# Kernel optimization log

Hardware: AMD Instinct MI355X
Metric: run time of the kernel (lower is better)

## Reference

```python
import jax, jax.numpy as jnp
import numpy as np

B, T, DIM = 1, 1024, 1024
H = 8
QLR, KVLR = 768, 512
DNOPE, DROPE, DV = 128, 64, 128
DK = DNOPE + DROPE  # 192
EPS = 1e-5


def _rms(x, w):
    return x * jax.lax.rsqrt(jnp.mean(x * x, axis=-1, keepdims=True) + EPS) * w


def _l2norm(x):
    return x * jax.lax.rsqrt(jnp.sum(x * x, axis=-1, keepdims=True) + 1e-6)


def setup_inputs() -> dict:
    key = jax.random.key(0)
    ks = jax.random.split(key, 12)
    std = 0.02
    rnd = lambda k, shape: (jax.random.normal(k, shape, dtype=jnp.float32) * std)
    return {
        'x': jax.random.normal(ks[0], (B, T, DIM), dtype=jnp.float32),
        'cos': jax.random.normal(ks[1], (T, DROPE), dtype=jnp.float32),
        'sin': jax.random.normal(ks[2], (T, DROPE), dtype=jnp.float32),
        'wq_a': rnd(ks[3], (DIM, QLR)),
        'q_norm_w': jnp.ones((QLR,), dtype=jnp.float32),
        'wq_b': rnd(ks[4], (QLR, H * DK)),
        'wkv_a': rnd(ks[5], (DIM, KVLR + DROPE)),
        'kv_norm_w': jnp.ones((KVLR,), dtype=jnp.float32),
        'wkv_b': rnd(ks[6], (KVLR, H * (DNOPE + DV))),
        'wg_w': rnd(ks[7], (DIM, H * DK)),
        'wg_b': jnp.zeros((H * DK,), dtype=jnp.float32),
        'wb': rnd(ks[8], (DIM, H)),
        'wo': rnd(ks[9], (H * DV, DIM)),
    }


def _kda(q, k, v, g, beta):
    # q,k: [B,T,H,DK]; v: [B,T,H,DV]; g: [B,T,H,DK] (log-decay); beta: [B,T,H]
    q = _l2norm(q) * (DK ** -0.5)
    k = _l2norm(k)
    # time-major for scan
    qs = jnp.moveaxis(q, 1, 0)
    ks_ = jnp.moveaxis(k, 1, 0)
    vs = jnp.moveaxis(v, 1, 0)
    gs = jnp.moveaxis(g, 1, 0)
    bs = jnp.moveaxis(beta, 1, 0)

    def step(S, inp):
        q_t, k_t, v_t, g_t, b_t = inp  # [B,H,DK],[B,H,DK],[B,H,DV],[B,H,DK],[B,H]
        S = S * jnp.exp(g_t)[..., None]                       # per-key-dim decay
        u_t = b_t[..., None] * (v_t - jnp.einsum('bhk,bhkv->bhv', k_t, S))
        S = S + k_t[..., None] * u_t[..., None, :]            # rank-1 delta update
        o_t = jnp.einsum('bhk,bhkv->bhv', q_t, S)
        return S, o_t

    S0 = jnp.zeros((B, H, DK, DV), dtype=q.dtype)
    _, o = jax.lax.scan(step, S0, (qs, ks_, vs, gs, bs))
    return jnp.moveaxis(o, 0, 1)  # [B,T,H,DV]


def reference(x, cos, sin, wq_a, q_norm_w, wq_b, wkv_a, kv_norm_w, wkv_b, wg_w, wg_b, wb, wo):
    # cos/sin are accepted but unused, matching the original forward body.
    q = (_rms(x @ wq_a, q_norm_w) @ wq_b).reshape(B, T, H, DK)
    kv_all = x @ wkv_a
    kv_c, k_pe = kv_all[..., :KVLR], kv_all[..., KVLR:]       # [B,T,KVLR],[B,T,DROPE]
    kv = (_rms(kv_c, kv_norm_w) @ wkv_b).reshape(B, T, H, DNOPE + DV)
    k_nope, v = kv[..., :DNOPE], kv[..., DNOPE:]
    k = jnp.concatenate(
        [k_nope, jnp.broadcast_to(k_pe[:, :, None, :], (B, T, H, DROPE))], axis=-1)
    g = jax.nn.log_sigmoid(x @ wg_w + wg_b).reshape(B, T, H, DK)
    beta = jax.nn.sigmoid(x @ wb).reshape(B, T, H)
    o = _kda(q, k, v, g, beta)
    o = jnp.nan_to_num(o, nan=0.0, posinf=10000.0, neginf=-10000.0)
    return o.reshape(B, T, H * DV) @ wo
```

## Files before the change

### kernel.cpp

```cpp
#include <hip/hip_runtime.h>
#include <hip/hip_bf16.h>
#include <math.h>

#define TT 1024
#define DIM 1024
#define HH 8
#define QLR 768
#define KVLR 512
#define DNOPE 128
#define DROPE 64
#define DV 128
#define DK 192
#define HDK (HH*DK)
#define HKV (HH*(DNOPE+DV))

#define OY   0
#define OQ   3072
#define OC   6144
#define OPL  9984
#define OU   10240
#define OLAM 12288
#define PABLK 12480

typedef __attribute__((ext_vector_type(8))) short short8;
typedef __attribute__((ext_vector_type(4))) float f32x4;

__device__ __forceinline__ unsigned short f2bf_rn(float f) {
    unsigned u = __float_as_uint(f);
    unsigned lsb = (u >> 16) & 1u;
    u += 0x7fffu + lsb;
    return (unsigned short)(u >> 16);
}
__device__ __forceinline__ float bf2f(unsigned short h) {
    return __uint_as_float(((unsigned)h) << 16);
}

__global__ __launch_bounds__(256) void wconv(
    const float* __restrict__ W0, unsigned short* __restrict__ H0,
    unsigned short* __restrict__ L0, int K0, int N0, int T0,
    const float* __restrict__ W1, unsigned short* __restrict__ H1,
    unsigned short* __restrict__ L1, int K1, int N1, int T1,
    const float* __restrict__ W2, unsigned short* __restrict__ H2,
    unsigned short* __restrict__ L2, int K2, int N2, int T2)
{
    __shared__ float Ls[64][65];
    int bx = blockIdx.x;
    const float* W; unsigned short* H; unsigned short* L; int K, N;
    if (bx < T0)           { W = W0; H = H0; L = L0; K = K0; N = N0; }
    else if (bx < T0 + T1) { bx -= T0; W = W1; H = H1; L = L1; K = K1; N = N1; }
    else                   { bx -= T0 + T1; W = W2; H = H2; L = L2; K = K2; N = N2; }

    const int NT = N >> 6;
    const int kt = bx / NT, nt = bx - kt * NT;
    const int k0 = kt * 64, n0 = nt * 64;
    const int tid = threadIdx.x;
    const int r = tid >> 2, c = (tid & 3) * 16;

#pragma unroll
    for (int i = 0; i < 4; i++)
        *(float4*)&Ls[r][c + i * 4] =
            *(const float4*)&W[(size_t)(k0 + r) * N + n0 + c + i * 4];
    __syncthreads();

    const int nr = tid >> 2, kc = (tid & 3) * 16;
    unsigned short hb[16], lb[16];
#pragma unroll
    for (int j = 0; j < 16; j++) {
        float v = Ls[kc + j][nr];
        unsigned short h = f2bf_rn(v);
        hb[j] = h;
        lb[j] = f2bf_rn(v - bf2f(h));
    }
    size_t ob = (size_t)(n0 + nr) * K + k0 + kc;
    *(float4*)&H[ob]     = ((float4*)hb)[0];
    *(float4*)&H[ob + 8] = ((float4*)hb)[1];
    *(float4*)&L[ob]     = ((float4*)lb)[0];
    *(float4*)&L[ob + 8] = ((float4*)lb)[1];
}

__global__ __launch_bounds__(256) void aconv(
    const float* __restrict__ A, unsigned short* __restrict__ H,
    unsigned short* __restrict__ L)
{
    int i = (blockIdx.x * 256 + threadIdx.x) * 8;
    float4 v0 = *(const float4*)&A[i];
    float4 v1 = *(const float4*)&A[i + 4];
    float vv[8] = {v0.x, v0.y, v0.z, v0.w, v1.x, v1.y, v1.z, v1.w};
    unsigned short hb[8], lb[8];
#pragma unroll
    for (int j = 0; j < 8; j++) {
        unsigned short h = f2bf_rn(vv[j]);
        hb[j] = h;
        lb[j] = f2bf_rn(vv[j] - bf2f(h));
    }
    *(float4*)&H[i] = *(float4*)hb;
    *(float4*)&L[i] = *(float4*)lb;
}

__global__ __launch_bounds__(128) void gemm_bt(
    const unsigned short* __restrict__ Ah0, const unsigned short* __restrict__ Al0,
    const unsigned short* __restrict__ Bh0, const unsigned short* __restrict__ Bl0,
    float* __restrict__ C0, int K0, int N0, int T0,
    const unsigned short* __restrict__ Ah1, const unsigned short* __restrict__ Al1,
    const unsigned short* __restrict__ Bh1, const unsigned short* __restrict__ Bl1,
    float* __restrict__ C1, int K1, int N1, int T1,
    const unsigned short* __restrict__ Ah2, const unsigned short* __restrict__ Al2,
    const unsigned short* __restrict__ Bh2, const unsigned short* __restrict__ Bl2,
    float* __restrict__ C2, int K2, int N2, int T2)
{
    __shared__ unsigned short Ahs[64 * 40], Als[64 * 40];
    __shared__ unsigned short Bhs[64 * 40], Bls[64 * 40];

    int bx = blockIdx.x;
    const unsigned short *Ah, *Al, *Bh, *Bl; float* C; int K, N;
    if (bx < T0) {
        Ah = Ah0; Al = Al0; Bh = Bh0; Bl = Bl0; C = C0; K = K0; N = N0;
    } else if (bx < T0 + T1) {
        bx -= T0; Ah = Ah1; Al = Al1; Bh = Bh1; Bl = Bl1; C = C1; K = K1; N = N1;
    } else {
        bx -= T0 + T1; Ah = Ah2; Al = Al2; Bh = Bh2; Bl = Bl2; C = C2; K = K2; N = N2;
    }

    const int tid = threadIdx.x;
    const int w = tid >> 6, l = tid & 63;
    const int q = l >> 4, m16 = l & 15;
    const int bm = blockIdx.y * 64, bn = bx * 64;

    const int c0i = tid * 2, c1i = tid * 2 + 1;
    const int r0 = c0i >> 2, o0 = (c0i & 3) * 8;
    const int r1 = c1i >> 2, o1 = (c1i & 3) * 8;
    const unsigned short* pAh0 = Ah + (size_t)(bm + r0) * K + o0;
    const unsigned short* pAh1 = Ah + (size_t)(bm + r1) * K + o1;
    const unsigned short* pAl0 = Al + (size_t)(bm + r0) * K + o0;
    const unsigned short* pAl1 = Al + (size_t)(bm + r1) * K + o1;
    const unsigned short* pBh0 = Bh + (size_t)(bn + r0) * K + o0;
    const unsigned short* pBh1 = Bh + (size_t)(bn + r1) * K + o1;
    const unsigned short* pBl0 = Bl + (size_t)(bn + r0) * K + o0;
    const unsigned short* pBl1 = Bl + (size_t)(bn + r1) * K + o1;

    f32x4 acc[2][4];
#pragma unroll
    for (int i = 0; i < 2; i++)
#pragma unroll
        for (int j = 0; j < 4; j++)
            acc[i][j] = (f32x4){0.f, 0.f, 0.f, 0.f};

    float4 vAh0 = *(const float4*)pAh0, vAh1 = *(const float4*)pAh1;
    float4 vAl0 = *(const float4*)pAl0, vAl1 = *(const float4*)pAl1;
    float4 vBh0 = *(const float4*)pBh0, vBh1 = *(const float4*)pBh1;
    float4 vBl0 = *(const float4*)pBl0, vBl1 = *(const float4*)pBl1;

    for (int k0 = 0;; k0 += 32) {
        __syncthreads();
        *(float4*)&Ahs[r0 * 40 + o0] = vAh0; *(float4*)&Ahs[r1 * 40 + o1] = vAh1;
        *(float4*)&Als[r0 * 40 + o0] = vAl0; *(float4*)&Als[r1 * 40 + o1] = vAl1;
        *(float4*)&Bhs[r0 * 40 + o0] = vBh0; *(float4*)&Bhs[r1 * 40 + o1] = vBh1;
        *(float4*)&Bls[r0 * 40 + o0] = vBl0; *(float4*)&Bls[r1 * 40 + o1] = vBl1;
        __syncthreads();

        const bool more = (k0 + 32) < K;
        if (more) {
            const int kn = k0 + 32;
            vAh0 = *(const float4*)(pAh0 + kn); vAh1 = *(const float4*)(pAh1 + kn);
            vAl0 = *(const float4*)(pAl0 + kn); vAl1 = *(const float4*)(pAl1 + kn);
            vBh0 = *(const float4*)(pBh0 + kn); vBh1 = *(const float4*)(pBh1 + kn);
            vBl0 = *(const float4*)(pBl0 + kn); vBl1 = *(const float4*)(pBl1 + kn);
        }

        short8 fah[2], fal[2], fbh[4], fbl[4];
#pragma unroll
        for (int mt = 0; mt < 2; mt++) {
            const int row = w * 32 + mt * 16 + m16;
            fah[mt] = *(const short8*)&Ahs[row * 40 + q * 8];
            fal[mt] = *(const short8*)&Als[row * 40 + q * 8];
        }
#pragma unroll
        for (int nt = 0; nt < 4; nt++) {
            const int row = nt * 16 + m16;
            fbh[nt] = *(const short8*)&Bhs[row * 40 + q * 8];
            fbl[nt] = *(const short8*)&Bls[row * 40 + q * 8];
        }
#pragma unroll
        for (int mt = 0; mt < 2; mt++)
#pragma unroll
            for (int nt = 0; nt < 4; nt++) {
                acc[mt][nt] = __builtin_amdgcn_mfma_f32_16x16x32_bf16(
                    fah[mt], fbh[nt], acc[mt][nt], 0, 0, 0);
                acc[mt][nt] = __builtin_amdgcn_mfma_f32_16x16x32_bf16(
                    fah[mt], fbl[nt], acc[mt][nt], 0, 0, 0);
                acc[mt][nt] = __builtin_amdgcn_mfma_f32_16x16x32_bf16(
                    fal[mt], fbh[nt], acc[mt][nt], 0, 0, 0);
            }
        if (!more) break;
    }

#pragma unroll
    for (int mt = 0; mt < 2; mt++)
#pragma unroll
        for (int nt = 0; nt < 4; nt++) {
            const int mrow = bm + w * 32 + mt * 16 + q * 4;
            const int ncol = bn + nt * 16 + m16;
#pragma unroll
            for (int r = 0; r < 4; r++)
                C[(size_t)(mrow + r) * N + ncol] = acc[mt][nt][r];
        }
}

__global__ __launch_bounds__(256) void rmsnorm_bf(
    const float* __restrict__ in, int in_stride, const float* __restrict__ w,
    unsigned short* __restrict__ oh, unsigned short* __restrict__ ol,
    int ncols, float inv_n)
{
    const int t = blockIdx.x;
    const int tid = threadIdx.x;
    const float* row = in + (size_t)t * in_stride;
    float ss = 0.f;
    for (int c = tid; c < ncols; c += 256) { float v = row[c]; ss += v * v; }
#pragma unroll
    for (int m = 1; m < 64; m <<= 1) ss += __shfl_xor(ss, m);
    __shared__ float red[4];
    if ((tid & 63) == 0) red[tid >> 6] = ss;
    __syncthreads();
    float tot = red[0] + red[1] + red[2] + red[3];
    float scale = rsqrtf(tot * inv_n + 1e-5f);
    for (int c = tid; c < ncols; c += 256) {
        float v = row[c] * scale * w[c];
        unsigned short h = f2bf_rn(v);
        oh[(size_t)t * ncols + c] = h;
        ol[(size_t)t * ncols + c] = f2bf_rn(v - bf2f(h));
    }
}

__global__ __launch_bounds__(256) void logsig_relayout(
    const float* __restrict__ g, const float* __restrict__ bias,
    float* __restrict__ la_h)
{
    int i = blockIdx.x * 256 + threadIdx.x;
    int t = i / HDK, col = i - t * HDK;
    int h = col / DK, d = col - h * DK;
    float z = g[i] + bias[col];
    float la = fminf(z, 0.f) - log1pf(__expf(-fabsf(z)));
    la_h[((size_t)h * TT + t) * DK + d] = la;
}

__global__ __launch_bounds__(256) void beta_kernel(
    const float* __restrict__ x, const float* __restrict__ wb,
    float* __restrict__ beta)
{
    const int lane = threadIdx.x & 63, wv = threadIdx.x >> 6;
    const int p = blockIdx.x * 4 + wv;
    const int t = p >> 3, h = p & 7;
    const float* xr = x + (size_t)t * DIM;
    float s = 0.f;
    for (int e = lane; e < DIM; e += 64) s += xr[e] * wb[e * HH + h];
#pragma unroll
    for (int m = 1; m < 64; m <<= 1) s += __shfl_xor(s, m);
    if (lane == 0) beta[p] = 1.f / (1.f + expf(-s));
}

__global__ __launch_bounds__(256) void prep_qk(
    const float* __restrict__ qraw, const float* __restrict__ kvb,
    const float* __restrict__ kv_all, float* __restrict__ q_h,
    float* __restrict__ k_h)
{
    const int lane = threadIdx.x & 63, wv = threadIdx.x >> 6;
    const int p = blockIdx.x * 4 + wv;
    const int t = p >> 3, h = p & 7;

    const float* qrow = qraw + (size_t)t * HDK + h * DK;
    float q0 = qrow[lane], q1 = qrow[lane + 64], q2 = qrow[lane + 128];
    float ss = q0 * q0 + q1 * q1 + q2 * q2;
#pragma unroll
    for (int m = 1; m < 64; m <<= 1) ss += __shfl_xor(ss, m);
    float sc = rsqrtf(ss + 1e-6f) * 0.07216878364870323f;
    float* qo = q_h + ((size_t)h * TT + t) * DK;
    qo[lane] = q0 * sc; qo[lane + 64] = q1 * sc; qo[lane + 128] = q2 * sc;

    const float* knope = kvb + (size_t)t * HKV + h * (DNOPE + DV);
    float k0 = knope[lane], k1 = knope[lane + 64];
    float k2 = kv_all[(size_t)t * (KVLR + DROPE) + KVLR + lane];
    float ks = k0 * k0 + k1 * k1 + k2 * k2;
#pragma unroll
    for (int m = 1; m < 64; m <<= 1) ks += __shfl_xor(ks, m);
    float kc = rsqrtf(ks + 1e-6f);
    float* ko = k_h + ((size_t)h * TT + t) * DK;
    ko[lane] = k0 * kc; ko[lane + 64] = k1 * kc; ko[lane + 128] = k2 * kc;
}

__device__ __forceinline__ float dpp_xor1(float x) {
    return __int_as_float(__builtin_amdgcn_update_dpp(
        0, __float_as_int(x), 0xB1, 0xF, 0xF, false));
}
__device__ __forceinline__ float dpp_xor2(float x) {
    return __int_as_float(__builtin_amdgcn_update_dpp(
        0, __float_as_int(x), 0x4E, 0xF, 0xF, false));
}
__device__ __forceinline__ float red16(float x) {
    x += dpp_xor1(x);
    x += dpp_xor2(x);
    x += __int_as_float(__builtin_amdgcn_update_dpp(0, __float_as_int(x), 0x141, 0xF, 0xF, false));
    x += __int_as_float(__builtin_amdgcn_update_dpp(0, __float_as_int(x), 0x140, 0xF, 0xF, false));
    return x;
}

__device__ __forceinline__ void gl_lds16(const float* g, float* l) {
    __builtin_amdgcn_global_load_lds(
        (const __attribute__((address_space(1))) void*)g,
        (__attribute__((address_space(3))) void*)l, 16, 0, 0);
}
__device__ __forceinline__ void gl_lds4(const float* g, float* l) {
    __builtin_amdgcn_global_load_lds(
        (const __attribute__((address_space(1))) void*)g,
        (__attribute__((address_space(3))) void*)l, 4, 0, 0);
}

__global__ __launch_bounds__(256) void chunk_prep(
    const float* __restrict__ k_h, const float* __restrict__ la_h,
    const float* __restrict__ q_h, const float* __restrict__ kvb,
    const float* __restrict__ betab, float* __restrict__ pa)
{
    __shared__ float Ls[16][196];
    __shared__ float Ks[16][196];
    __shared__ float Qs[16][196];
    __shared__ float Ws[16][196];
    __shared__ float Xs[16][196];
    __shared__ float Ms[16][16];
    __shared__ float bs[16];

    const int tid = threadIdx.x;
    const int n = blockIdx.x >> 3, h = blockIdx.x & 7;
    const size_t g0 = ((size_t)h * TT + n * 16) * DK;
    float* blob = pa + (size_t)blockIdx.x * PABLK;

#pragma unroll
    for (int s = 0; s < 3; s++) {
        int off = (tid * 3 + s) * 4;
        int r = off / 192, c = off - r * 192;
        *(float4*)&Ks[r][c] = *(const float4*)(k_h + g0 + off);
        *(float4*)&Ls[r][c] = *(const float4*)(la_h + g0 + off);
        *(float4*)&Qs[r][c] = *(const float4*)(q_h + g0 + off);
    }
    if (tid < 16) bs[tid] = betab[(size_t)(n * 16 + tid) * HH + h];
    __syncthreads();

    if (tid < 192) {
        float g = 0.f;
#pragma unroll
        for (int i = 0; i < 16; i++) { g += Ls[i][tid]; Ls[i][tid] = g; }
    }
    __syncthreads();

#pragma unroll
    for (int s = 0; s < 12; s++) {
        int idx = s * 256 + tid;
        int i = idx / 192, d = idx - i * 192;
        float G = Ls[i][d];
        float eg = __expf(G), en = __expf(-G);
        float kk = Ks[i][d];
        Ws[i][d] = bs[i] * kk * eg;
        Qs[i][d] *= eg;
        Ks[i][d] = kk * en;
    }
    __syncthreads();

#pragma unroll
    for (int s = 0; s < 3; s++) {
        int off = (tid * 3 + s) * 4;
        int r = off / 192, c = off - r * 192;
        *(float4*)(blob + OQ + off) = *(const float4*)&Qs[r][c];
    }
    if (tid < 192) {
        float lam = __expf(Ls[15][tid]);
        blob[OLAM + tid] = lam;
#pragma unroll
        for (int j4 = 0; j4 < 4; j4++) {
            float4 v;
            v.x = Ks[j4 * 4 + 0][tid] * lam; v.y = Ks[j4 * 4 + 1][tid] * lam;
            v.z = Ks[j4 * 4 + 2][tid] * lam; v.w = Ks[j4 * 4 + 3][tid] * lam;
            *(float4*)(blob + OC + tid * 20 + j4 * 4) = v;
        }
        blob[OC + tid * 20 + 16] = 0.f; blob[OC + tid * 20 + 17] = 0.f;
        blob[OC + tid * 20 + 18] = 0.f; blob[OC + tid * 20 + 19] = 0.f;
    }
    {
        const int i = tid >> 4, j = tid & 15;
        float m = 0.f, p = 0.f;
#pragma unroll
        for (int d4 = 0; d4 < 48; d4++) {
            float4 w  = *(const float4*)&Ws[i][d4 * 4];
            float4 ka = *(const float4*)&Ks[j][d4 * 4];
            float4 qa = *(const float4*)&Qs[i][d4 * 4];
            m += w.x * ka.x + w.y * ka.y + w.z * ka.z + w.w * ka.w;
            p += qa.x * ka.x + qa.y * ka.y + qa.z * ka.z + qa.w * ka.w;
        }
        Ms[i][j] = (j < i) ? m : 0.f;
        blob[OPL + tid] = (j <= i) ? p : 0.f;
    }
    __syncthreads();

    float y[16], uu[16];
    const bool doY = (tid < 192);
    const bool doU = (tid >= 128);
    const int dcol = tid, ccol = tid - 128;
    if (doY) {
#pragma unroll
        for (int i = 0; i < 16; i++) y[i] = Ws[i][dcol];
#pragma unroll
        for (int i = 1; i < 16; i++)
#pragma unroll
            for (int j = 0; j < i; j++)
                y[i] = fmaf(-Ms[i][j], y[j], y[i]);
    }
    if (doU) {
#pragma unroll
        for (int i = 0; i < 16; i++)
            uu[i] = bs[i] * kvb[(size_t)(n * 16 + i) * HKV + h * (DNOPE + DV) + DNOPE + ccol];
#pragma unroll
        for (int i = 1; i < 16; i++)
#pragma unroll
            for (int j = 0; j < i; j++)
                uu[i] = fmaf(-Ms[i][j], uu[j], uu[i]);
    }
    if (doY) {
#pragma unroll
        for (int i = 0; i < 16; i++) Xs[i][dcol] = y[i];
    }
    __syncthreads();
#pragma unroll
    for (int s = 0; s < 3; s++) {
        int off = (tid * 3 + s) * 4;
        int r = off / 192, c = off - r * 192;
        *(float4*)(blob + OY + off) = *(const float4*)&Xs[r][c];
    }
    __syncthreads();
    if (doU) {
#pragma unroll
        for (int i = 0; i < 16; i++) Xs[i][ccol] = uu[i];
    }
    __syncthreads();
#pragma unroll
    for (int s = 0; s < 2; s++) {
        int off = (tid * 2 + s) * 4;
        int r = off / 128, c = off - r * 128;
        *(float4*)(blob + OU + off) = *(const float4*)&Xs[r][c];
    }
}

__global__ __launch_bounds__(256) void kda_chunk(
    const float* __restrict__ pa, unsigned short* __restrict__ obh,
    unsigned short* __restrict__ obl)
{
    __shared__ float Yb[3][3136];
    __shared__ float Qb[3][3136];
    __shared__ float Cb[3][3840];
    __shared__ float Pb[3][256];
    __shared__ float ubs[3][64];
    __shared__ float lbs[3][192];
    __shared__ float Ss[784];
    __shared__ float us[80];

    const int tid = threadIdx.x;
    const int w = tid >> 6, lane = tid & 63;
    const int h = blockIdx.x >> 5, cg = blockIdx.x & 31;
    const int c0 = cg * 4;

    const int dg  = tid & 15;
    const int ccg = (tid >> 4) & 1;
    const int tig = tid >> 5;

    auto stage = [&](int buf, int n) {
        const float* blob = pa + (size_t)(n * 8 + h) * PABLK;
        if (w == 0) {
            if (lane < 48)
#pragma unroll
                for (int r = 0; r < 16; r++)
                    gl_lds16(blob + OY + r * 192 + lane * 4, &Yb[buf][r * 196]);
        } else if (w == 1) {
            if (lane < 48)
#pragma unroll
                for (int r = 0; r < 16; r++)
                    gl_lds16(blob + OQ + r * 192 + lane * 4, &Qb[buf][r * 196]);
        } else if (w == 2) {
#pragma unroll
            for (int s = 0; s < 15; s++)
                gl_lds16(blob + OC + s * 256 + lane * 4, &Cb[buf][s * 256]);
        } else {
            gl_lds16(blob + OPL + lane * 4, &Pb[buf][0]);
            gl_lds4(blob + OU + (lane >> 2) * 128 + c0 + (lane & 3), &ubs[buf][0]);
            if (lane < 48)
                gl_lds16(blob + OLAM + lane * 4, &lbs[buf][0]);
        }
    };

    for (int idx = tid; idx < 784; idx += 256) Ss[idx] = 0.f;
    stage(0, 0);
    stage(1, 1);

    const int c2 = tid & 3, dseg = tid >> 2;

    int buf = 0;
    for (int n = 0; n < TT / 16; n++) {
        __syncthreads();

        if (n + 2 < TT / 16) {
            int b2 = buf + 2; if (b2 >= 3) b2 -= 3;
            stage(b2, n + 2);
        }

        const int dbase = dg * 12;
        float4 sv[2][3];
#pragma unroll
        for (int j = 0; j < 2; j++)
#pragma unroll
            for (int s = 0; s < 3; s++)
                sv[j][s] = *(const float4*)&Ss[(ccg * 2 + j) * 196 + dbase + s * 4];

        float py[2][2] = {{0.f, 0.f}, {0.f, 0.f}};
        float pq[2][2] = {{0.f, 0.f}, {0.f, 0.f}};
#pragma unroll
        for (int i = 0; i < 2; i++) {
            const float* Yr = &Yb[buf][(tig * 2 + i) * 196 + dbase];
            const float* Qr = &Qb[buf][(tig * 2 + i) * 196 + dbase];
#pragma unroll
            for (int s = 0; s < 3; s++) {
                float4 yv = *(const float4*)(Yr + s * 4);
                float4 qv = *(const float4*)(Qr + s * 4);
#pragma unroll
                for (int j = 0; j < 2; j++) {
                    float4 s4 = sv[j][s];
                    py[i][j] = fmaf(yv.x, s4.x, py[i][j]);
                    py[i][j] = fmaf(yv.y, s4.y, py[i][j]);
                    py[i][j] = fmaf(yv.z, s4.z, py[i][j]);
                    py[i][j] = fmaf(yv.w, s4.w, py[i][j]);
                    pq[i][j] = fmaf(qv.x, s4.x, pq[i][j]);
                    pq[i][j] = fmaf(qv.y, s4.y, pq[i][j]);
                    pq[i][j] = fmaf(qv.z, s4.z, pq[i][j]);
                    pq[i][j] = fmaf(qv.w, s4.w, pq[i][j]);
                }
            }
        }
        float zy[2][2], zq[2][2];
#pragma unroll
        for (int i = 0; i < 2; i++)
#pragma unroll
            for (int j = 0; j < 2; j++) {
                zy[i][j] = red16(py[i][j]);
                zq[i][j] = red16(pq[i][j]);
            }

        float uv[2][2];
#pragma unroll
        for (int i = 0; i < 2; i++)
#pragma unroll
            for (int j = 0; j < 2; j++)
                uv[i][j] = ubs[buf][(tig * 2 + i) * 4 + (ccg * 2 + j)] - zy[i][j];
        {
            const int m = dg >> 2;
            if ((dg & 3) == 0) {
                const int ii = m >> 1, jj = m & 1;
                float val = (m == 0) ? uv[0][0] : (m == 1) ? uv[0][1]
                          : (m == 2) ? uv[1][0] : uv[1][1];
                us[(ccg * 2 + jj) * 20 + (tig * 2 + ii)] = val;
            }
        }
        __syncthreads();

        {
            const int m = dg >> 2, qtr = dg & 3;
            const int ii = m >> 1, jj = m & 1;
            const int ti = tig * 2 + ii, cc = ccg * 2 + jj;
            float acc = 0.f;
            for (int j = qtr; j <= ti; j += 4)
                acc = fmaf(Pb[buf][ti * 16 + j], us[cc * 20 + j], acc);
            acc += dpp_xor1(acc);
            acc += dpp_xor2(acc);
            if (qtr == 0) {
                float zqv = (m == 0) ? zq[0][0] : (m == 1) ? zq[0][1]
                          : (m == 2) ? zq[1][0] : zq[1][1];
                float ov = zqv + acc;
                if (isnan(ov)) ov = 0.f;
                else if (isinf(ov)) ov = ov > 0.f ? 1e4f : -1e4f;
                size_t oi = (size_t)(n * 16 + ti) * (HH * DV) + h * DV + c0 + cc;
                unsigned short hb = f2bf_rn(ov);
                obh[oi] = hb;
                obl[oi] = f2bf_rn(ov - bf2f(hb));
            }
        }

        const float4* up = (const float4*)&us[c2 * 20];
        float4 u0 = up[0], u1 = up[1], u2v = up[2], u3 = up[3];
#pragma unroll
        for (int s = 0; s < 3; s++) {
            int d = dseg * 3 + s;
            float svv = Ss[c2 * 196 + d];
            float a2 = lbs[buf][d] * svv;
            const float4* C4 = (const float4*)&Cb[buf][d * 20];
            float4 k0 = C4[0], k1 = C4[1], k2 = C4[2], k3 = C4[3];
            a2 = fmaf(k0.x, u0.x,  a2); a2 = fmaf(k0.y, u0.y,  a2);
            a2 = fmaf(k0.z, u0.z,  a2); a2 = fmaf(k0.w, u0.w,  a2);
            a2 = fmaf(k1.x, u1.x,  a2); a2 = fmaf(k1.y, u1.y,  a2);
            a2 = fmaf(k1.z, u1.z,  a2); a2 = fmaf(k1.w, u1.w,  a2);
            a2 = fmaf(k2.x, u2v.x, a2); a2 = fmaf(k2.y, u2v.y, a2);
            a2 = fmaf(k2.z, u2v.z, a2); a2 = fmaf(k2.w, u2v.w, a2);
            a2 = fmaf(k3.x, u3.x,  a2); a2 = fmaf(k3.y, u3.y,  a2);
            a2 = fmaf(k3.z, u3.z,  a2); a2 = fmaf(k3.w, u3.w,  a2);
            Ss[c2 * 196 + d] = a2;
        }
        buf = (buf + 1 == 3) ? 0 : buf + 1;
    }
}

extern "C" void kernel_launch(void* const* d_in, const int* in_sizes, int n_in,
                              void* d_out, int out_size, void* d_ws, size_t ws_size,
                              hipStream_t stream)
{
    const float* x         = (const float*)d_in[0];
    const float* wq_a      = (const float*)d_in[3];
    const float* q_norm_w  = (const float*)d_in[4];
    const float* wq_b      = (const float*)d_in[5];
    const float* wkv_a     = (const float*)d_in[6];
    const float* kv_norm_w = (const float*)d_in[7];
    const float* wkv_b     = (const float*)d_in[8];
    const float* wg_w      = (const float*)d_in[9];
    const float* wg_b      = (const float*)d_in[10];
    const float* wb        = (const float*)d_in[11];
    const float* wo        = (const float*)d_in[12];
    float* out = (float*)d_out;

    float* ws = (float*)d_ws;
    float* xq     = ws;
    float* kv_all = xq     + TT * QLR;
    float* agraw  = kv_all + TT * (KVLR + DROPE);
    float* qnraw  = agraw  + TT * HDK;
    float* kvb    = qnraw  + TT * HDK;
    float* la_h   = kvb    + TT * HKV;
    float* q_h    = la_h   + TT * HDK;
    float* k_h    = q_h    + TT * HDK;
    float* betab  = k_h    + TT * HDK;
    float* pa     = betab  + TT * HH;
    float* tail   = pa     + 512 * PABLK;

    unsigned short* wo_h  = (unsigned short*)tail;
    unsigned short* wo_l  = wo_h  + 1048576;
    unsigned short* xh    = wo_l  + 1048576;
    unsigned short* xl    = xh    + 1048576;
    unsigned short* xqh   = xl    + 1048576;
    unsigned short* xql   = xqh   + 786432;
    unsigned short* kvnh  = xql   + 786432;
    unsigned short* kvnl  = kvnh  + 524288;

    unsigned short* wqa_h  = (unsigned short*)pa;
    unsigned short* wqa_l  = wqa_h  + 786432;
    unsigned short* wkva_h = wqa_l  + 786432;
    unsigned short* wkva_l = wkva_h + 589824;
    unsigned short* wgw_h  = wkva_l + 589824;
    unsigned short* wgw_l  = wgw_h  + 1572864;
    unsigned short* wqb_h  = wgw_l  + 1572864;
    unsigned short* wqb_l  = wqb_h  + 1179648;
    unsigned short* wkvb_h = wqb_l  + 1179648;
    unsigned short* wkvb_l = wkvb_h + 1048576;

    unsigned short* obh = (unsigned short*)agraw;
    unsigned short* obl = obh + 1048576;

    dim3 blk(256);

    wconv<<<dim3(192 + 144 + 384), blk, 0, stream>>>(
        wq_a, wqa_h, wqa_l, DIM, QLR, 192,
        wkv_a, wkva_h, wkva_l, DIM, KVLR + DROPE, 144,
        wg_w, wgw_h, wgw_l, DIM, HDK, 384);
    wconv<<<dim3(288 + 256 + 256), blk, 0, stream>>>(
        wq_b, wqb_h, wqb_l, QLR, HDK, 288,
        wkv_b, wkvb_h, wkvb_l, KVLR, HKV, 256,
        wo, wo_h, wo_l, DIM, DIM, 256);

    aconv<<<dim3(TT * DIM / (256 * 8)), blk, 0, stream>>>(x, xh, xl);

    gemm_bt<<<dim3(12 + 9 + 24, 16), dim3(128), 0, stream>>>(
        xh, xl, wqa_h, wqa_l, xq, DIM, QLR, 12,
        xh, xl, wkva_h, wkva_l, kv_all, DIM, KVLR + DROPE, 9,
        xh, xl, wgw_h, wgw_l, agraw, DIM, HDK, 24);

    rmsnorm_bf<<<TT, blk, 0, stream>>>(xq, QLR, q_norm_w, xqh, xql, QLR, 1.f / QLR);
    rmsnorm_bf<<<TT, blk, 0, stream>>>(kv_all, KVLR + DROPE, kv_norm_w, kvnh, kvnl, KVLR, 1.f / KVLR);

    gemm_bt<<<dim3(24 + 32, 16), dim3(128), 0, stream>>>(
        xqh, xql, wqb_h, wqb_l, qnraw, QLR, HDK, 24,
        kvnh, kvnl, wkvb_h, wkvb_l, kvb, KVLR, HKV, 32,
        xh, xl, wqa_h, wqa_l, xq, DIM, QLR, 0);

    logsig_relayout<<<(TT * HDK + 255) / 256, blk, 0, stream>>>(agraw, wg_b, la_h);
    beta_kernel<<<TT * HH / 4, blk, 0, stream>>>(x, wb, betab);

    prep_qk<<<TT * HH / 4, blk, 0, stream>>>(qnraw, kvb, kv_all, q_h, k_h);

    chunk_prep<<<512, blk, 0, stream>>>(k_h, la_h, q_h, kvb, betab, pa);
    kda_chunk<<<256, blk, 0, stream>>>(pa, obh, obl);

    gemm_bt<<<dim3(16, 16), dim3(128), 0, stream>>>(
        obh, obl, wo_h, wo_l, out, DIM, DIM, 16,
        xh, xl, wqa_h, wqa_l, xq, DIM, QLR, 0,
        xh, xl, wqa_h, wqa_l, xq, DIM, QLR, 0);
}
```

Measured before the change: 326.1 us.

## Merge small launches and stream Y/Q chunk data through registers in kda_chunk

Result: no change. 320.8 us (-1.6%).

```diff
diff --git a/kernel.cpp b/kernel.cpp
--- a/kernel.cpp
+++ b/kernel.cpp
@@ -206,14 +206,24 @@
         }
 }
 
-__global__ __launch_bounds__(256) void rmsnorm_bf(
-    const float* __restrict__ in, int in_stride, const float* __restrict__ w,
-    unsigned short* __restrict__ oh, unsigned short* __restrict__ ol,
-    int ncols, float inv_n)
+__global__ __launch_bounds__(256) void rmsnorm_bf2(
+    const float* __restrict__ in0, const float* __restrict__ w0,
+    unsigned short* __restrict__ oh0, unsigned short* __restrict__ ol0,
+    const float* __restrict__ in1, const float* __restrict__ w1,
+    unsigned short* __restrict__ oh1, unsigned short* __restrict__ ol1)
 {
-    const int t = blockIdx.x;
+    int bx = blockIdx.x;
+    const float* in; const float* w; unsigned short *oh, *ol;
+    int t, stride, ncols; float inv_n;
+    if (bx < TT) {
+        t = bx; in = in0; w = w0; oh = oh0; ol = ol0;
+        stride = QLR; ncols = QLR; inv_n = 1.f / QLR;
+    } else {
+        t = bx - TT; in = in1; w = w1; oh = oh1; ol = ol1;
+        stride = KVLR + DROPE; ncols = KVLR; inv_n = 1.f / KVLR;
+    }
     const int tid = threadIdx.x;
-    const float* row = in + (size_t)t * in_stride;
+    const float* row = in + (size_t)t * stride;
     float ss = 0.f;
     for (int c = tid; c < ncols; c += 256) { float v = row[c]; ss += v * v; }
 #pragma unroll
@@ -231,60 +241,62 @@
     }
 }
 
-__global__ __launch_bounds__(256) void logsig_relayout(
+__global__ __launch_bounds__(256) void small_fused(
     const float* __restrict__ g, const float* __restrict__ bias,
-    float* __restrict__ la_h)
-{
-    int i = blockIdx.x * 256 + threadIdx.x;
-    int t = i / HDK, col = i - t * HDK;
-    int h = col / DK, d = col - h * DK;
-    float z = g[i] + bias[col];
-    float la = fminf(z, 0.f) - log1pf(__expf(-fabsf(z)));
-    la_h[((size_t)h * TT + t) * DK + d] = la;
-}
-
-__global__ __launch_bounds__(256) void beta_kernel(
+    float* __restrict__ la_h,
     const float* __restrict__ x, const float* __restrict__ wb,
-    float* __restrict__ beta)
-{
-    const int lane = threadIdx.x & 63, wv = threadIdx.x >> 6;
-    const int p = blockIdx.x * 4 + wv;
-    const int t = p >> 3, h = p & 7;
-    const float* xr = x + (size_t)t * DIM;
-    float s = 0.f;
-    for (int e = lane; e < DIM; e += 64) s += xr[e] * wb[e * HH + h];
-#pragma unroll
-    for (int m = 1; m < 64; m <<= 1) s += __shfl_xor(s, m);
-    if (lane == 0) beta[p] = 1.f / (1.f + expf(-s));
-}
-
-__global__ __launch_bounds__(256) void prep_qk(
+    float* __restrict__ betab,
     const float* __restrict__ qraw, const float* __restrict__ kvb,
     const float* __restrict__ kv_all, float* __restrict__ q_h,
     float* __restrict__ k_h)
 {
+    int bx = blockIdx.x;
+    if (bx < 6144) {
+        int i = bx * 256 + threadIdx.x;
+        int t = i / HDK, col = i - t * HDK;
+        int h = col / DK, d = col - h * DK;
+        float z = g[i] + bias[col];
+        float la = fminf(z, 0.f) - log1pf(__expf(-fabsf(z)));
+        la_h[((size_t)h * TT + t) * DK + d] = la;
+        return;
+    }
+    bx -= 6144;
     const int lane = threadIdx.x & 63, wv = threadIdx.x >> 6;
-    const int p = blockIdx.x * 4 + wv;
-    const int t = p >> 3, h = p & 7;
-
-    const float* qrow = qraw + (size_t)t * HDK + h * DK;
-    float q0 = qrow[lane], q1 = qrow[lane + 64], q2 = qrow[lane + 128];
-    float ss = q0 * q0 + q1 * q1 + q2 * q2;
-#pragma unroll
-    for (int m = 1; m < 64; m <<= 1) ss += __shfl_xor(ss, m);
-    float sc = rsqrtf(ss + 1e-6f) * 0.07216878364870323f;
-    float* qo = q_h + ((size_t)h * TT + t) * DK;
-    qo[lane] = q0 * sc; qo[lane + 64] = q1 * sc; qo[lane + 128] = q2 * sc;
-
-    const float* knope = kvb + (size_t)t * HKV + h * (DNOPE + DV);
-    float k0 = knope[lane], k1 = knope[lane + 64];
-    float k2 = kv_all[(size_t)t * (KVLR + DROPE) + KVLR + lane];
-    float ks = k0 * k0 + k1 * k1 + k2 * k2;
-#pragma unroll
-    for (int m = 1; m < 64; m <<= 1) ks += __shfl_xor(ks, m);
-    float kc = rsqrtf(ks + 1e-6f);
-    float* ko = k_h + ((size_t)h * TT + t) * DK;
-    ko[lane] = k0 * kc; ko[lane + 64] = k1 * kc; ko[lane + 128] = k2 * kc;
+    if (bx < 2048) {
+        const int p = bx * 4 + wv;
+        const int t = p >> 3, h = p & 7;
+        const float* xr = x + (size_t)t * DIM;
+        float s = 0.f;
+        for (int e = lane; e < DIM; e += 64) s += xr[e] * wb[e * HH + h];
+#pragma unroll
+        for (int m = 1; m < 64; m <<= 1) s += __shfl_xor(s, m);
+        if (lane == 0) betab[p] = 1.f / (1.f + expf(-s));
+        return;
+    }
+    bx -= 2048;
+    {
+        const int p = bx * 4 + wv;
+        const int t = p >> 3, h = p & 7;
+
+        const float* qrow = qraw + (size_t)t * HDK + h * DK;
+        float q0 = qrow[lane], q1 = qrow[lane + 64], q2 = qrow[lane + 128];
+        float ss = q0 * q0 + q1 * q1 + q2 * q2;
+#pragma unroll
+        for (int m = 1; m < 64; m <<= 1) ss += __shfl_xor(ss, m);
+        float sc = rsqrtf(ss + 1e-6f) * 0.07216878364870323f;
+        float* qo = q_h + ((size_t)h * TT + t) * DK;
+        qo[lane] = q0 * sc; qo[lane + 64] = q1 * sc; qo[lane + 128] = q2 * sc;
+
+        const float* knope = kvb + (size_t)t * HKV + h * (DNOPE + DV);
+        float k0 = knope[lane], k1 = knope[lane + 64];
+        float k2 = kv_all[(size_t)t * (KVLR + DROPE) + KVLR + lane];
+        float ks = k0 * k0 + k1 * k1 + k2 * k2;
+#pragma unroll
+        for (int m = 1; m < 64; m <<= 1) ks += __shfl_xor(ks, m);
+        float kc = rsqrtf(ks + 1e-6f);
+        float* ko = k_h + ((size_t)h * TT + t) * DK;
+        ko[lane] = k0 * kc; ko[lane + 64] = k1 * kc; ko[lane + 128] = k2 * kc;
+    }
 }
 
 __device__ __forceinline__ float dpp_xor1(float x) {
@@ -450,8 +462,6 @@
     const float* __restrict__ pa, unsigned short* __restrict__ obh,
     unsigned short* __restrict__ obl)
 {
-    __shared__ float Yb[3][3136];
-    __shared__ float Qb[3][3136];
     __shared__ float Cb[3][3840];
     __shared__ float Pb[3][256];
     __shared__ float ubs[3][64];
@@ -467,24 +477,19 @@
     const int dg  = tid & 15;
     const int ccg = (tid >> 4) & 1;
     const int tig = tid >> 5;
+    const int dbase = dg * 12;
 
     auto stage = [&](int buf, int n) {
         const float* blob = pa + (size_t)(n * 8 + h) * PABLK;
         if (w == 0) {
-            if (lane < 48)
-#pragma unroll
-                for (int r = 0; r < 16; r++)
-                    gl_lds16(blob + OY + r * 192 + lane * 4, &Yb[buf][r * 196]);
+#pragma unroll
+            for (int s = 0; s < 8; s++)
+                gl_lds16(blob + OC + s * 256 + lane * 4, &Cb[buf][s * 256]);
         } else if (w == 1) {
-            if (lane < 48)
-#pragma unroll
-                for (int r = 0; r < 16; r++)
-                    gl_lds16(blob + OQ + r * 192 + lane * 4, &Qb[buf][r * 196]);
+#pragma unroll
+            for (int s = 8; s < 15; s++)
+                gl_lds16(blob + OC + s * 256 + lane * 4, &Cb[buf][s * 256]);
         } else if (w == 2) {
-#pragma unroll
-            for (int s = 0; s < 15; s++)
-                gl_lds16(blob + OC + s * 256 + lane * 4, &Cb[buf][s * 256]);
-        } else {
             gl_lds16(blob + OPL + lane * 4, &Pb[buf][0]);
             gl_lds4(blob + OU + (lane >> 2) * 128 + c0 + (lane & 3), &ubs[buf][0]);
             if (lane < 48)
@@ -492,22 +497,42 @@
         }
     };
 
+    auto ldYQ = [&](int n, float4 (&Y)[2][3], float4 (&Q)[2][3]) {
+        const float* blob = pa + (size_t)(n * 8 + h) * PABLK;
+#pragma unroll
+        for (int i = 0; i < 2; i++) {
+            const float* py = blob + OY + (tig * 2 + i) * 192 + dbase;
+            const float* pq = blob + OQ + (tig * 2 + i) * 192 + dbase;
+#pragma unroll
+            for (int s = 0; s < 3; s++) {
+                Y[i][s] = *(const float4*)(py + s * 4);
+                Q[i][s] = *(const float4*)(pq + s * 4);
+            }
+        }
+    };
+
     for (int idx = tid; idx < 784; idx += 256) Ss[idx] = 0.f;
     stage(0, 0);
     stage(1, 1);
 
+    float4 YA[2][3], QA[2][3], YB[2][3], QB[2][3];
+    ldYQ(0, YA, QA);
+
     const int c2 = tid & 3, dseg = tid >> 2;
 
-    int buf = 0;
-    for (int n = 0; n < TT / 16; n++) {
+    auto body = [&](int n, int bf, float4 (&Yc)[2][3], float4 (&Qc)[2][3],
+                    float4 (&Yn)[2][3], float4 (&Qn)[2][3]) {
         __syncthreads();
 
         if (n + 2 < TT / 16) {
-            int b2 = buf + 2; if (b2 >= 3) b2 -= 3;
+            int b2 = bf + 2; if (b2 >= 3) b2 -= 3;
             stage(b2, n + 2);
         }
-
-        const int dbase = dg * 12;
+        {
+            int np = n + 1; if (np > TT / 16 - 1) np = TT / 16 - 1;
+            ldYQ(np, Yn, Qn);
+        }
+
         float4 sv[2][3];
 #pragma unroll
         for (int j = 0; j < 2; j++)
@@ -518,13 +543,11 @@
         float py[2][2] = {{0.f, 0.f}, {0.f, 0.f}};
         float pq[2][2] = {{0.f, 0.f}, {0.f, 0.f}};
 #pragma unroll
-        for (int i = 0; i < 2; i++) {
-            const float* Yr = &Yb[buf][(tig * 2 + i) * 196 + dbase];
-            const float* Qr = &Qb[buf][(tig * 2 + i) * 196 + dbase];
+        for (int i = 0; i < 2; i++)
 #pragma unroll
             for (int s = 0; s < 3; s++) {
-                float4 yv = *(const float4*)(Yr + s * 4);
-                float4 qv = *(const float4*)(Qr + s * 4);
+                float4 yv = Yc[i][s];
+                float4 qv = Qc[i][s];
 #pragma unroll
                 for (int j = 0; j < 2; j++) {
                     float4 s4 = sv[j][s];
@@ -538,7 +561,6 @@
                     pq[i][j] = fmaf(qv.w, s4.w, pq[i][j]);
                 }
             }
-        }
         float zy[2][2], zq[2][2];
 #pragma unroll
         for (int i = 0; i < 2; i++)
@@ -553,7 +575,7 @@
         for (int i = 0; i < 2; i++)
 #pragma unroll
             for (int j = 0; j < 2; j++)
-                uv[i][j] = ubs[buf][(tig * 2 + i) * 4 + (ccg * 2 + j)] - zy[i][j];
+                uv[i][j] = ubs[bf][(tig * 2 + i) * 4 + (ccg * 2 + j)] - zy[i][j];
         {
             const int m = dg >> 2;
             if ((dg & 3) == 0) {
@@ -571,7 +593,7 @@
             const int ti = tig * 2 + ii, cc = ccg * 2 + jj;
             float acc = 0.f;
             for (int j = qtr; j <= ti; j += 4)
-                acc = fmaf(Pb[buf][ti * 16 + j], us[cc * 20 + j], acc);
+                acc = fmaf(Pb[bf][ti * 16 + j], us[cc * 20 + j], acc);
             acc += dpp_xor1(acc);
             acc += dpp_xor2(acc);
             if (qtr == 0) {
@@ -593,8 +615,8 @@
         for (int s = 0; s < 3; s++) {
             int d = dseg * 3 + s;
             float svv = Ss[c2 * 196 + d];
-            float a2 = lbs[buf][d] * svv;
-            const float4* C4 = (const float4*)&Cb[buf][d * 20];
+            float a2 = lbs[bf][d] * svv;
+            const float4* C4 = (const float4*)&Cb[bf][d * 20];
             float4 k0 = C4[0], k1 = C4[1], k2 = C4[2], k3 = C4[3];
             a2 = fmaf(k0.x, u0.x,  a2); a2 = fmaf(k0.y, u0.y,  a2);
             a2 = fmaf(k0.z, u0.z,  a2); a2 = fmaf(k0.w, u0.w,  a2);
@@ -606,7 +628,14 @@
             a2 = fmaf(k3.z, u3.z,  a2); a2 = fmaf(k3.w, u3.w,  a2);
             Ss[c2 * 196 + d] = a2;
         }
-        buf = (buf + 1 == 3) ? 0 : buf + 1;
+    };
+
+    int buf = 0;
+    for (int n = 0; n < TT / 16; n += 2) {
+        body(n, buf, YA, QA, YB, QB);
+        int b1 = buf + 1; if (b1 >= 3) b1 -= 3;
+        body(n + 1, b1, YB, QB, YA, QA);
+        buf += 2; if (buf >= 3) buf -= 3;
     }
 }
 
@@ -681,18 +710,19 @@
         xh, xl, wkva_h, wkva_l, kv_all, DIM, KVLR + DROPE, 9,
         xh, xl, wgw_h, wgw_l, agraw, DIM, HDK, 24);
 
-    rmsnorm_bf<<<TT, blk, 0, stream>>>(xq, QLR, q_norm_w, xqh, xql, QLR, 1.f / QLR);
-    rmsnorm_bf<<<TT, blk, 0, stream>>>(kv_all, KVLR + DROPE, kv_norm_w, kvnh, kvnl, KVLR, 1.f / KVLR);
+    rmsnorm_bf2<<<dim3(2 * TT), blk, 0, stream>>>(
+        xq, q_norm_w, xqh, xql,
+        kv_all, kv_norm_w, kvnh, kvnl);
 
     gemm_bt<<<dim3(24 + 32, 16), dim3(128), 0, stream>>>(
         xqh, xql, wqb_h, wqb_l, qnraw, QLR, HDK, 24,
         kvnh, kvnl, wkvb_h, wkvb_l, kvb, KVLR, HKV, 32,
         xh, xl, wqa_h, wqa_l, xq, DIM, QLR, 0);
 
-    logsig_relayout<<<(TT * HDK + 255) / 256, blk, 0, stream>>>(agraw, wg_b, la_h);
-    beta_kernel<<<TT * HH / 4, blk, 0, stream>>>(x, wb, betab);
-
-    prep_qk<<<TT * HH / 4, blk, 0, stream>>>(qnraw, kvb, kv_all, q_h, k_h);
+    small_fused<<<dim3(6144 + 2048 + 2048), blk, 0, stream>>>(
+        agraw, wg_b, la_h,
+        x, wb, betab,
+        qnraw, kvb, kv_all, q_h, k_h);
 
     chunk_prep<<<512, blk, 0, stream>>>(k_h, la_h, q_h, kvb, betab, pa);
     kda_chunk<<<256, blk, 0, stream>>>(pa, obh, obl);
```
